# Optimization experiments

Hardware: AMD Instinct MI355X
Metric: run time of the kernel (lower is better)

## Reference

```python
import jax, jax.numpy as jnp
import numpy as np
import math

DIM, H, Q_RANK, KV_RANK = 2048, 16, 768, 512
QK_STATIC, QK_ROT, V_DIM = 128, 64, 128
QK_TOTAL = QK_STATIC + QK_ROT
BS, SEQ = 2, 1024


def rmsnorm(x, scale, eps=1e-6):
    xf = x.astype(jnp.float32)
    return scale * (xf * jax.lax.rsqrt(jnp.mean(xf * xf, axis=-1, keepdims=True) + eps))


def half_rotate(x):
    h = x.shape[-1] // 2
    return jnp.concatenate([-x[..., h:], x[..., :h]], axis=-1)


def rope_tables(seq_len, dim):
    inv_freq = 1.0 / (10000.0 ** (jnp.arange(0, dim, 2, dtype=jnp.float32) / dim))
    freqs = jnp.arange(seq_len, dtype=jnp.float32)[:, None] * inv_freq[None, :]
    cos = jnp.concatenate([jnp.cos(freqs), jnp.cos(freqs)], axis=-1)  # (S, dim)
    sin = jnp.concatenate([jnp.sin(freqs), jnp.sin(freqs)], axis=-1)
    return cos, sin


def setup_inputs() -> dict:
    key = jax.random.key(0)
    ks = jax.random.split(key, 10)
    sc = lambda fan_in: 1.0 / math.sqrt(fan_in)
    x = jax.random.normal(ks[0], (BS, SEQ, DIM), dtype=jnp.float32)
    causal = jnp.where(jnp.tril(jnp.ones((SEQ, SEQ), dtype=bool)), 0.0, -1e9).astype(jnp.float32)
    mask = jnp.broadcast_to(causal[None], (BS, SEQ, SEQ))
    return {
        "x": x,
        "start_pos": 0,
        "mask": mask,
        "q_down_w": jax.random.normal(ks[1], (Q_RANK, DIM)) * sc(DIM),
        "q_down_b": jnp.zeros((Q_RANK,), jnp.float32),
        "q_norm_scale": jnp.ones((Q_RANK,), jnp.float32),
        "q_up_w": jax.random.normal(ks[2], (H * QK_TOTAL, Q_RANK)) * sc(Q_RANK),
        "q_up_b": jnp.zeros((H * QK_TOTAL,), jnp.float32),
        "kv_down_w": jax.random.normal(ks[3], (KV_RANK + QK_ROT, DIM)) * sc(DIM),
        "kv_down_b": jnp.zeros((KV_RANK + QK_ROT,), jnp.float32),
        "kv_norm_scale": jnp.ones((KV_RANK,), jnp.float32),
        "kv_up_w": jax.random.normal(ks[4], (H * (QK_STATIC + V_DIM), KV_RANK)) * sc(KV_RANK),
        "out_w": jax.random.normal(ks[5], (DIM, H * V_DIM)) * sc(H * V_DIM),
        "out_b": jnp.zeros((DIM,), jnp.float32),
    }


def reference(x, start_pos, mask, q_down_w, q_down_b, q_norm_scale, q_up_w, q_up_b,
              kv_down_w, kv_down_b, kv_norm_scale, kv_up_w, out_w, out_b):
    bs, seq_len, _ = x.shape
    # q path: down-proj -> RMSNorm -> up-proj
    q = rmsnorm(x @ q_down_w.T + q_down_b, q_norm_scale)
    q = (q @ q_up_w.T + q_up_b).reshape(bs, seq_len, H, QK_TOTAL)
    q_static, q_rot = q[..., :QK_STATIC], q[..., QK_STATIC:]
    # kv path: shared down-proj producing latent features + rotary key part
    kv = x @ kv_down_w.T + kv_down_b
    kv_feat, k_rot = kv[..., :KV_RANK], kv[..., KV_RANK:]
    # RoPE (original indexes positions 0..seq_len-1)
    cos, sin = rope_tables(seq_len, QK_ROT)
    q_rot = q_rot * cos[None, :, None, :] + half_rotate(q_rot) * sin[None, :, None, :]
    k_rot = k_rot * cos[None, :, :] + half_rotate(k_rot) * sin[None, :, :]  # (b, t, r)
    kv_normed = rmsnorm(kv_feat, kv_norm_scale)  # latent cache contents (b, t, c)
    # matrix absorption: fold kv_up key-weights into q
    w_k_abs = kv_up_w[: H * QK_STATIC, :].reshape(H, QK_STATIC, KV_RANK)
    w_v_abs = kv_up_w[-H * V_DIM :, :].reshape(H, V_DIM, KV_RANK)
    q_static_proj = jnp.einsum('bshd,hdc->bshc', q_static, w_k_abs)
    attn_scores = (jnp.einsum('bshc,btc->bsht', q_static_proj, kv_normed)
                   + jnp.einsum('bshr,btr->bsht', q_rot, k_rot)) / math.sqrt(QK_TOTAL)
    attn_scores = attn_scores + mask[:, :, None, :]
    attn_weights = jax.nn.softmax(attn_scores, axis=-1)
    # attend over latent features, then expand with absorbed value weights
    ctx_c = jnp.einsum('bsht,btc->bshc', attn_weights, kv_normed)
    ctx = jnp.einsum('bshc,hdc->bshd', ctx_c, w_v_abs)
    out = ctx.reshape(bs, seq_len, H * V_DIM) @ out_w.T + out_b
    return out
```

## Files before the change

kernel.cpp:

```cpp
#include <hip/hip_runtime.h>
#include <stdint.h>
#include <stddef.h>


typedef __attribute__((ext_vector_type(8))) short bf16x8;
typedef __attribute__((ext_vector_type(4))) float f32x4;

__device__ inline float b2f(unsigned short v){
    union { unsigned u; float f; } x; x.u = ((unsigned)v) << 16; return x.f;
}
__device__ inline unsigned short f2b(float f){
    union { float f; unsigned u; } x; x.f = f;
    unsigned r = x.u + 0x7fffu + ((x.u >> 16) & 1u);
    return (unsigned short)(r >> 16);
}
__device__ inline float tofloat(float v){ return v; }
__device__ inline float tofloat(unsigned short v){ return b2f(v); }

__device__ __forceinline__ void gl2lds16(const unsigned short* g, unsigned short* l){
    __builtin_amdgcn_global_load_lds(
        (__attribute__((address_space(1))) void*)const_cast<unsigned short*>(g),
        (__attribute__((address_space(3))) void*)l,
        16, 0, 0);
}

template<typename TC>
__global__ __launch_bounds__(256) void mfma_gemm_bt(
    const unsigned short* __restrict__ A, const unsigned short* __restrict__ B,
    const float* __restrict__ bias, TC* __restrict__ C,
    int M, int N, int K, int lda, int ldb, int ldc,
    int zdiv, long sA_hi, long sA_lo, long sB_hi, long sB_lo, long sC_hi, long sC_lo,
    float alpha, int causal)
{
    int z, bm, bn;
    if (causal & 4){ z = blockIdx.x; bm = blockIdx.y; bn = blockIdx.z; }
    else           { z = blockIdx.z; bm = blockIdx.y; bn = blockIdx.x; }
    int m0, n0;
    if (causal & 1){
        int i = bm;
        int mt = (int)((sqrtf(8.f * i + 1.f) - 1.f) * 0.5f);
        while ((mt + 1) * (mt + 2) / 2 <= i) ++mt;
        while (mt * (mt + 1) / 2 > i) --mt;
        n0 = (i - mt * (mt + 1) / 2) * 128;
        m0 = mt * 128;
    } else { m0 = bm * 128; n0 = bn * 128; }
    if (causal & 2) K = min(K, m0 + 128);

    __shared__ unsigned short As[3][4096];
    __shared__ unsigned short Bs[3][4096];
    const int zh = z / zdiv, zl = z % zdiv;
    A += (size_t)zh * sA_hi + (size_t)zl * sA_lo;
    B += (size_t)zh * sB_hi + (size_t)zl * sB_lo;
    C += (size_t)zh * sC_hi + (size_t)zl * sC_lo;

    const int tid = threadIdx.x, w = tid >> 6, lane = tid & 63;
    const int wm = w >> 1, wn = w & 1;

    const int srow = w * 32 + (lane >> 2);
    const int schunk = ((lane & 3) ^ ((lane >> 3) & 3)) * 8;
    const unsigned short* gA = A + (size_t)(m0 + srow) * lda + schunk;
    const unsigned short* gB = B + (size_t)(n0 + srow) * ldb + schunk;

    const int ktiles = K >> 5;
    auto stage = [&](int buf, int kt){
        const int k0 = kt << 5;
        gl2lds16(gA + k0,            &As[buf][w * 1024]);
        gl2lds16(gA + k0 + 16 * lda, &As[buf][w * 1024 + 512]);
        gl2lds16(gB + k0,            &Bs[buf][w * 1024]);
        gl2lds16(gB + k0 + 16 * ldb, &Bs[buf][w * 1024 + 512]);
    };
    stage(0, 0);
    if (ktiles > 1) stage(1, 1);

    f32x4 acc[4][4] = {};
    const int lm = lane & 15;
    const int kq = (((lane >> 4) ^ (lm >> 1)) & 3) * 8;

    int cur = 0;
    for (int kt = 0; kt < ktiles; ++kt){
        if (kt + 1 < ktiles) __builtin_amdgcn_s_waitcnt(0xF74);
        else                 __builtin_amdgcn_s_waitcnt(0xF70);
        __builtin_amdgcn_s_barrier();
        __asm__ volatile("" ::: "memory");
        if (kt + 2 < ktiles) stage(cur >= 1 ? cur - 1 : 2, kt + 2);
        bf16x8 af[4], bfr[4];
        #pragma unroll
        for (int i = 0; i < 4; ++i)
            af[i] = *(const bf16x8*)&As[cur][(wm * 64 + i * 16 + lm) * 32 + kq];
        #pragma unroll
        for (int j = 0; j < 4; ++j)
            bfr[j] = *(const bf16x8*)&Bs[cur][(wn * 64 + j * 16 + lm) * 32 + kq];
        #pragma unroll
        for (int i = 0; i < 4; ++i)
            #pragma unroll
            for (int j = 0; j < 4; ++j)
                acc[i][j] = __builtin_amdgcn_mfma_f32_16x16x32_bf16(af[i], bfr[j], acc[i][j], 0, 0, 0);
        __asm__ volatile("" ::: "memory");
        cur = (cur == 2) ? 0 : cur + 1;
    }

    #pragma unroll
    for (int i = 0; i < 4; ++i){
        const int m = m0 + wm * 64 + i * 16 + (lane >> 4) * 4;
        #pragma unroll
        for (int j = 0; j < 4; ++j){
            const int n = n0 + wn * 64 + j * 16 + lm;
            if (n < N){
                const float bb = bias ? bias[n] : 0.f;
                #pragma unroll
                for (int r = 0; r < 4; ++r){
                    float v = acc[i][j][r] * alpha + bb;
                    if ((causal & 1) && n > m + r) v = -1e9f;
                    if constexpr (sizeof(TC) == 2)
                        C[(size_t)(m + r) * ldc + n] = (TC)f2b(v);
                    else
                        C[(size_t)(m + r) * ldc + n] = (TC)v;
                }
            }
        }
    }
}

__global__ __launch_bounds__(256) void flash_attn(
    const unsigned short* __restrict__ qcat,
    const unsigned short* __restrict__ kcat,
    const unsigned short* __restrict__ vhT,
    unsigned short* __restrict__ ctx)
{
    const int z = blockIdx.x;
    const int mt = 15 - (int)blockIdx.y;
    const int b = z >> 4, h = z & 15;
    const int m0 = mt * 64;
    const int nkt = (mt >> 1) + 1;

    __shared__ char smem[74240];
    unsigned short (*Qs)[4096] = (unsigned short (*)[4096])smem;
    unsigned short (*Ks)[8192] = (unsigned short (*)[8192])(smem + 24576);
    unsigned short* Ps = (unsigned short*)smem;
    float* lrow = (float*)(smem + 73728);

    const unsigned short* qA = qcat + ((size_t)b * 16384 + h) * 576;
    const unsigned short* kB = kcat + (size_t)b * 589824;
    const unsigned short* vB = vhT + (size_t)z * 131072;

    const int tid = threadIdx.x, w = tid >> 6, lane = tid & 63;
    const int wm = w >> 1, wn = w & 1;
    const int lm = lane & 15, g = lane >> 4;
    const int kq = g * 8;
    const int rs7 = lm & 7;

    if (tid < 128) lrow[tid] = 0.f;

    const int srow8 = lane >> 3;
    const int soff8 = ((lane & 7) ^ (lane >> 3)) * 8;
    const unsigned short* gQ = qA + (size_t)(m0 + w * 16 + srow8) * 9216 + soff8;

    f32x4 Oacc[2][4] = {};
    const float scl = 0.07216878364870322f;

    for (int kt = 0; kt < nkt; ++kt){
        bf16x8 vfr[4][4];
        #pragma unroll
        for (int j = 0; j < 4; ++j)
            #pragma unroll
            for (int kc = 0; kc < 4; ++kc)
                vfr[j][kc] = *(const bf16x8*)(vB + (size_t)(wn * 64 + j * 16 + lm) * 1024
                                              + kt * 128 + kc * 32 + kq);

        const unsigned short* gK = kB + (size_t)(kt * 128 + w * 32 + srow8) * 576 + soff8;
        auto stageQK = [&](int buf, int c){
            const int k0 = c * 64;
            gl2lds16(gQ + k0,             &Qs[buf][w * 1024]);
            gl2lds16(gQ + k0 + 8 * 9216,  &Qs[buf][w * 1024 + 512]);
            gl2lds16(gK + k0,             &Ks[buf][w * 2048]);
            gl2lds16(gK + k0 + 8 * 576,   &Ks[buf][w * 2048 + 512]);
            gl2lds16(gK + k0 + 16 * 576,  &Ks[buf][w * 2048 + 1024]);
            gl2lds16(gK + k0 + 24 * 576,  &Ks[buf][w * 2048 + 1536]);
        };
        stageQK(0, 0);
        stageQK(1, 1);

        f32x4 S[2][4] = {};
        int cur = 0;
        for (int c = 0; c < 9; ++c){
            if (c < 8) __builtin_amdgcn_s_waitcnt(0xF76);
            else       __builtin_amdgcn_s_waitcnt(0xF70);
            __builtin_amdgcn_s_barrier();
            __asm__ volatile("" ::: "memory");
            if (c + 2 < 9) stageQK(cur >= 1 ? cur - 1 : 2, c + 2);
            bf16x8 af[2][2], bfr[4][2];
            #pragma unroll
            for (int i = 0; i < 2; ++i)
                #pragma unroll
                for (int kk = 0; kk < 2; ++kk)
                    af[i][kk] = *(const bf16x8*)&Qs[cur][(wm * 32 + i * 16 + lm) * 64
                                                         + (((kk * 4 + g) ^ rs7) * 8)];
            #pragma unroll
            for (int j = 0; j < 4; ++j)
                #pragma unroll
                for (int kk = 0; kk < 2; ++kk)
                    bfr[j][kk] = *(const bf16x8*)&Ks[cur][(wn * 64 + j * 16 + lm) * 64
                                                          + (((kk * 4 + g) ^ rs7) * 8)];
            #pragma unroll
            for (int kk = 0; kk < 2; ++kk)
                #pragma unroll
                for (int i = 0; i < 2; ++i)
                    #pragma unroll
                    for (int j = 0; j < 4; ++j)
                        S[i][j] = __builtin_amdgcn_mfma_f32_16x16x32_bf16(af[i][kk], bfr[j][kk], S[i][j], 0, 0, 0);
            __asm__ volatile("" ::: "memory");
            cur = (cur == 2) ? 0 : cur + 1;
        }
        __syncthreads();

        const bool diag = (kt == (mt >> 1));
        #pragma unroll
        for (int i = 0; i < 2; ++i){
            float rs[4] = {0.f, 0.f, 0.f, 0.f};
            #pragma unroll
            for (int j = 0; j < 4; ++j){
                const int nloc = wn * 64 + j * 16 + lm;
                #pragma unroll
                for (int r = 0; r < 4; ++r){
                    const int mloc = wm * 32 + i * 16 + g * 4 + r;
                    float p = __expf(S[i][j][r] * scl);
                    if (diag && (kt * 128 + nloc) > (m0 + mloc)) p = 0.f;
                    rs[r] += p;
                    Ps[mloc * 136 + nloc] = f2b(p);
                }
            }
            #pragma unroll
            for (int r = 0; r < 4; ++r){
                rs[r] += __shfl_xor(rs[r], 1, 64);
                rs[r] += __shfl_xor(rs[r], 2, 64);
                rs[r] += __shfl_xor(rs[r], 4, 64);
                rs[r] += __shfl_xor(rs[r], 8, 64);
            }
            if (lm == 0){
                #pragma unroll
                for (int r = 0; r < 4; ++r)
                    lrow[wn * 64 + wm * 32 + i * 16 + g * 4 + r] += rs[r];
            }
        }
        __syncthreads();

        #pragma unroll
        for (int kc = 0; kc < 4; ++kc){
            bf16x8 pa[2];
            #pragma unroll
            for (int i = 0; i < 2; ++i)
                pa[i] = *(const bf16x8*)&Ps[(wm * 32 + i * 16 + lm) * 136 + kc * 32 + kq];
            #pragma unroll
            for (int i = 0; i < 2; ++i)
                #pragma unroll
                for (int j = 0; j < 4; ++j)
                    Oacc[i][j] = __builtin_amdgcn_mfma_f32_16x16x32_bf16(pa[i], vfr[j][kc], Oacc[i][j], 0, 0, 0);
        }
        __syncthreads();
    }

    unsigned short* cBase = ctx + ((size_t)(b * 1024 + m0)) * 2048 + h * 128;
    #pragma unroll
    for (int i = 0; i < 2; ++i){
        #pragma unroll
        for (int r = 0; r < 4; ++r){
            const int row = wm * 32 + i * 16 + g * 4 + r;
            const float inv = 1.f / (lrow[row] + lrow[64 + row]);
            #pragma unroll
            for (int j = 0; j < 4; ++j){
                const int col = wn * 64 + j * 16 + lm;
                cBase[(size_t)row * 2048 + col] = f2b(Oacc[i][j][r] * inv);
            }
        }
    }
}

__global__ __launch_bounds__(256) void cast_all(
    const float* __restrict__ s0, unsigned short* __restrict__ d0,
    const float* __restrict__ s1, unsigned short* __restrict__ d1,
    const float* __restrict__ s2, unsigned short* __restrict__ d2,
    const float* __restrict__ s3, unsigned short* __restrict__ d3,
    const float* __restrict__ s4, unsigned short* __restrict__ d4,
    const float* __restrict__ s5, unsigned short* __restrict__ d5)
{
    long i = (long)(blockIdx.x * 256 + threadIdx.x) * 4;
    const float* s; unsigned short* d; long off;
    if      (i <  4194304L){ s = s0; d = d0; off = i; }
    else if (i <  5767168L){ s = s1; d = d1; off = i -  4194304L; }
    else if (i <  8126464L){ s = s2; d = d2; off = i -  5767168L; }
    else if (i <  9306112L){ s = s3; d = d3; off = i -  8126464L; }
    else if (i < 11403264L){ s = s4; d = d4; off = i -  9306112L; }
    else                   { s = s5; d = d5; off = i - 11403264L; }
    float4 v = *(const float4*)(s + off);
    *(ushort4*)(d + off) = make_ushort4(f2b(v.x), f2b(v.y), f2b(v.z), f2b(v.w));
}

template<typename TIn>
__global__ __launch_bounds__(256) void transpose_to_bf16(
    const TIn* __restrict__ in, unsigned short* __restrict__ out,
    int ldin, int R, long sZin, long sZout)
{
    __shared__ float t[32][33];
    const int z = blockIdx.z;
    in  += (size_t)z * sZin;
    out += (size_t)z * sZout;
    const int r0 = blockIdx.y * 32, c0 = blockIdx.x * 32;
    const int tx = threadIdx.x & 31, ty = threadIdx.x >> 5;
    #pragma unroll
    for (int rr = ty; rr < 32; rr += 8)
        t[rr][tx] = tofloat(in[(size_t)(r0 + rr) * ldin + c0 + tx]);
    __syncthreads();
    #pragma unroll
    for (int cc = ty; cc < 32; cc += 8)
        out[(size_t)(c0 + cc) * R + r0 + tx] = f2b(t[tx][cc]);
}

__global__ __launch_bounds__(256) void fused_down_post(
    const unsigned short* __restrict__ p,
    const float* __restrict__ q_down_b, const float* __restrict__ kv_down_b,
    const float* __restrict__ q_norm_s, const float* __restrict__ kv_norm_s,
    unsigned short* __restrict__ qn, unsigned short* __restrict__ kcat)
{
    __shared__ float row[1344];
    __shared__ float red[4];
    const int t = blockIdx.x, tid = threadIdx.x;
    const long S = 2752512L;
    const unsigned short* b0 = p + (size_t)t * 1344;
    for (int c = tid; c < 1344; c += 256){
        float v = b2f(b0[c]) + b2f(b0[c + S]) + b2f(b0[c + 2*S]) + b2f(b0[c + 3*S]);
        v += (c < 768) ? q_down_b[c] : kv_down_b[c - 768];
        row[c] = v;
    }
    __syncthreads();
    const int lane = tid & 63, w = tid >> 6;
    float ss = 0.f;
    for (int c = tid; c < 768; c += 256){ float v = row[c]; ss += v * v; }
    #pragma unroll
    for (int o = 32; o > 0; o >>= 1) ss += __shfl_xor(ss, o, 64);
    if (lane == 0) red[w] = ss;
    __syncthreads();
    const float inv1 = rsqrtf((red[0]+red[1]+red[2]+red[3]) / 768.f + 1e-6f);
    __syncthreads();
    ss = 0.f;
    for (int c = tid; c < 512; c += 256){ float v = row[768 + c]; ss += v * v; }
    #pragma unroll
    for (int o = 32; o > 0; o >>= 1) ss += __shfl_xor(ss, o, 64);
    if (lane == 0) red[w] = ss;
    __syncthreads();
    const float inv2 = rsqrtf((red[0]+red[1]+red[2]+red[3]) / 512.f + 1e-6f);
    for (int c = tid; c < 768; c += 256)
        qn[(size_t)t * 768 + c] = f2b(q_norm_s[c] * row[c] * inv1);
    for (int c = tid; c < 512; c += 256)
        kcat[(size_t)t * 576 + c] = f2b(kv_norm_s[c] * row[768 + c] * inv2);
    if (tid < 64){
        const int d = tid, s = t & 1023;
        float x  = row[1280 + d];
        float xp = (d < 32) ? -row[1280 + d + 32] : row[1280 + d - 32];
        float ang = (float)s * powf(10000.f, -(float)(2 * (d & 31)) / 64.f);
        kcat[(size_t)t * 576 + 512 + d] = f2b(x * cosf(ang) + xp * sinf(ang));
    }
}

__global__ __launch_bounds__(256) void reduce_out(
    const unsigned short* __restrict__ p, const float* __restrict__ bias,
    float* __restrict__ out)
{
    const long S = 4194304L;
    long i = (long)(blockIdx.x * 256 + threadIdx.x) * 4;
    ushort4 a = *(const ushort4*)(p + i);
    ushort4 b = *(const ushort4*)(p + i + S);
    float4 bb = *(const float4*)(bias + (i & 2047));
    float4 r = make_float4(b2f(a.x) + b2f(b.x) + bb.x, b2f(a.y) + b2f(b.y) + bb.y,
                           b2f(a.z) + b2f(b.z) + bb.z, b2f(a.w) + b2f(b.w) + bb.w);
    *(float4*)(out + i) = r;
}

__global__ __launch_bounds__(256) void q_rope_kernel(const unsigned short* __restrict__ qu,
                                                     unsigned short* __restrict__ qcat)
{
    const int idx = blockIdx.x * 256 + threadIdx.x;
    const int d   = idx & 63;
    const int h   = (idx >> 6) & 15;
    const int tok = idx >> 10;
    const int s   = tok & 1023;
    const unsigned short* base = qu + (size_t)tok * 3072 + h * 192 + 128;
    float x  = b2f(base[d]);
    float xp = (d < 32) ? -b2f(base[d + 32]) : b2f(base[d - 32]);
    float ang = (float)s * powf(10000.f, -(float)(2 * (d & 31)) / 64.f);
    qcat[((size_t)tok * 16 + h) * 576 + 512 + d] = f2b(x * cosf(ang) + xp * sinf(ang));
}

extern "C" void kernel_launch(void* const* d_in, const int* in_sizes, int n_in,
                              void* d_out, int out_size, void* d_ws, size_t ws_size,
                              hipStream_t stream)
{
    const float* x         = (const float*)d_in[0];
    const float* q_down_w  = (const float*)d_in[3];
    const float* q_down_b  = (const float*)d_in[4];
    const float* q_norm_s  = (const float*)d_in[5];
    const float* q_up_w    = (const float*)d_in[6];
    const float* q_up_b    = (const float*)d_in[7];
    const float* kv_down_w = (const float*)d_in[8];
    const float* kv_down_b = (const float*)d_in[9];
    const float* kv_norm_s = (const float*)d_in[10];
    const float* kv_up_w   = (const float*)d_in[11];
    const float* out_w     = (const float*)d_in[12];
    const float* out_b     = (const float*)d_in[13];
    float* out = (float*)d_out;

    char* ws = (char*)d_ws;
    unsigned short* kvuw  = (unsigned short*)(ws + 0);
    unsigned short* outw  = (unsigned short*)(ws + 4194304);
    unsigned short* wkT   = (unsigned short*)(ws + 12582912);
    unsigned short* kcat  = (unsigned short*)(ws + 14680064);
    unsigned short* vhT   = (unsigned short*)(ws + 17039360);
    unsigned short* qcat  = (unsigned short*)(ws + 25427968);
    unsigned short* ctx   = (unsigned short*)(ws + 63176704);
    unsigned short* qu    = (unsigned short*)(ws + 71565312);
    unsigned short* qn    = (unsigned short*)(ws + 84148224);
    unsigned short* p_out = (unsigned short*)(ws + 71565312);
    unsigned short* p_qkv = (unsigned short*)(ws + 88342528);
    unsigned short* xb    = (unsigned short*)(ws + 110362624);
    unsigned short* qkdw  = (unsigned short*)(ws + 118751232);
    unsigned short* quw   = (unsigned short*)(ws + 124518400);

    dim3 blk(256);

    cast_all<<<15232, blk, 0, stream>>>(x, xb, q_down_w, qkdw, q_up_w, quw,
                                        kv_down_w, qkdw + 1572864, kv_up_w, kvuw, out_w, outw);
    transpose_to_bf16<float><<<dim3(16, 4, 16), blk, 0, stream>>>(
        kv_up_w, wkT, 512, 128, 65536L, 65536L);

    mfma_gemm_bt<unsigned short><<<dim3(11, 16, 4), blk, 0, stream>>>(
        xb, qkdw, nullptr, p_qkv, 2048, 1344, 512, 2048, 2048, 1344,
        4, 0L, 512L, 0L, 512L, 0L, 2752512L, 1.0f, 0);
    fused_down_post<<<2048, blk, 0, stream>>>(p_qkv, q_down_b, kv_down_b,
                                              q_norm_s, kv_norm_s, qn, kcat);
    mfma_gemm_bt<unsigned short><<<dim3(24, 16, 1), blk, 0, stream>>>(
        qn, quw, q_up_b, qu, 2048, 3072, 768, 768, 768, 3072,
        1, 0, 0, 0, 0, 0, 0, 1.0f, 0);
    mfma_gemm_bt<unsigned short><<<dim3(32, 1, 8), blk, 0, stream>>>(
        kvuw + 1048576, kcat, nullptr, vhT, 128, 1024, 512, 512, 576, 1024,
        16, 0L, 65536L, 589824L, 0L, 2097152L, 131072L, 1.0f, 4);
    q_rope_kernel<<<8192, blk, 0, stream>>>(qu, qcat);
    mfma_gemm_bt<unsigned short><<<dim3(16, 16, 4), blk, 0, stream>>>(
        qu, wkT, nullptr, qcat, 2048, 512, 128, 3072, 128, 9216,
        16, 0, 192L, 0, 65536L, 0, 576L, 1.0f, 4);
    flash_attn<<<dim3(32, 16), blk, 0, stream>>>(qcat, kcat, vhT, ctx);
    mfma_gemm_bt<unsigned short><<<dim3(16, 16, 2), blk, 0, stream>>>(
        ctx, outw, nullptr, p_out, 2048, 2048, 1024, 2048, 2048, 2048,
        2, 0L, 1024L, 0L, 1024L, 0L, 4194304L, 1.0f, 0);
    reduce_out<<<4096, blk, 0, stream>>>(p_out, out_b, out);
}
```

Measured before the change: 339.1 us.

## Un-absorb key weights: expand per-head K instead of projecting Q to latent

Instead of folding the key up-projection into Q (512-wide latent scores per head), the code now computes per-head keys K_h = kv_normed · W_k^T (128 dims) and concatenates the rotary part, so attention QK uses 192-dim dot products instead of 576. Q is read directly from the up-projection output with RoPE applied in place, and its three 64-wide chunks are loaded into LDS once per block rather than restaged every key tile. This removes the transpose kernel and the Q-absorption GEMM and cuts the QK MFMA work by about a third. In exchange it adds a per-head K expansion GEMM and a larger per-head key buffer, and the P tile now lives in the K staging region.

Measured after the change: 309.4 us. -8.8%, faster.

```diff
diff --git a/kernel.cpp b/kernel.cpp
--- a/kernel.cpp
+++ b/kernel.cpp
@@ -14,8 +14,6 @@
     unsigned r = x.u + 0x7fffu + ((x.u >> 16) & 1u);
     return (unsigned short)(r >> 16);
 }
-__device__ inline float tofloat(float v){ return v; }
-__device__ inline float tofloat(unsigned short v){ return b2f(v); }
 
 __device__ __forceinline__ void gl2lds16(const unsigned short* g, unsigned short* l){
     __builtin_amdgcn_global_load_lds(
@@ -122,8 +120,8 @@
 }
 
 __global__ __launch_bounds__(256) void flash_attn(
-    const unsigned short* __restrict__ qcat,
-    const unsigned short* __restrict__ kcat,
+    const unsigned short* __restrict__ qu,
+    const unsigned short* __restrict__ khcat,
     const unsigned short* __restrict__ vhT,
     unsigned short* __restrict__ ctx)
 {
@@ -136,11 +134,10 @@
     __shared__ char smem[74240];
     unsigned short (*Qs)[4096] = (unsigned short (*)[4096])smem;
     unsigned short (*Ks)[8192] = (unsigned short (*)[8192])(smem + 24576);
-    unsigned short* Ps = (unsigned short*)smem;
+    unsigned short* Ps = (unsigned short*)(smem + 24576);
     float* lrow = (float*)(smem + 73728);
 
-    const unsigned short* qA = qcat + ((size_t)b * 16384 + h) * 576;
-    const unsigned short* kB = kcat + (size_t)b * 589824;
+    const unsigned short* kB = khcat + (size_t)z * 196608;
     const unsigned short* vB = vhT + (size_t)z * 131072;
 
     const int tid = threadIdx.x, w = tid >> 6, lane = tid & 63;
@@ -153,7 +150,14 @@
 
     const int srow8 = lane >> 3;
     const int soff8 = ((lane & 7) ^ (lane >> 3)) * 8;
-    const unsigned short* gQ = qA + (size_t)(m0 + w * 16 + srow8) * 9216 + soff8;
+    const unsigned short* gQ = qu + (size_t)(b * 1024 + m0 + w * 16 + srow8) * 3072
+                               + h * 192 + soff8;
+
+    #pragma unroll
+    for (int c = 0; c < 3; ++c){
+        gl2lds16(gQ + c * 64,            &Qs[c][w * 1024]);
+        gl2lds16(gQ + c * 64 + 8 * 3072, &Qs[c][w * 1024 + 512]);
+    }
 
     f32x4 Oacc[2][4] = {};
     const float scl = 0.07216878364870322f;
@@ -167,40 +171,38 @@
                 vfr[j][kc] = *(const bf16x8*)(vB + (size_t)(wn * 64 + j * 16 + lm) * 1024
                                               + kt * 128 + kc * 32 + kq);
 
-        const unsigned short* gK = kB + (size_t)(kt * 128 + w * 32 + srow8) * 576 + soff8;
-        auto stageQK = [&](int buf, int c){
+        const unsigned short* gK = kB + (size_t)(kt * 128 + w * 32 + srow8) * 192 + soff8;
+        auto stageK = [&](int buf, int c){
             const int k0 = c * 64;
-            gl2lds16(gQ + k0,             &Qs[buf][w * 1024]);
-            gl2lds16(gQ + k0 + 8 * 9216,  &Qs[buf][w * 1024 + 512]);
-            gl2lds16(gK + k0,             &Ks[buf][w * 2048]);
-            gl2lds16(gK + k0 + 8 * 576,   &Ks[buf][w * 2048 + 512]);
-            gl2lds16(gK + k0 + 16 * 576,  &Ks[buf][w * 2048 + 1024]);
-            gl2lds16(gK + k0 + 24 * 576,  &Ks[buf][w * 2048 + 1536]);
+            gl2lds16(gK + k0,            &Ks[buf][w * 2048]);
+            gl2lds16(gK + k0 + 8 * 192,  &Ks[buf][w * 2048 + 512]);
+            gl2lds16(gK + k0 + 16 * 192, &Ks[buf][w * 2048 + 1024]);
+            gl2lds16(gK + k0 + 24 * 192, &Ks[buf][w * 2048 + 1536]);
         };
-        stageQK(0, 0);
-        stageQK(1, 1);
+        stageK(0, 0);
+        stageK(1, 1);
 
         f32x4 S[2][4] = {};
-        int cur = 0;
-        for (int c = 0; c < 9; ++c){
-            if (c < 8) __builtin_amdgcn_s_waitcnt(0xF76);
+        #pragma unroll
+        for (int c = 0; c < 3; ++c){
+            if (c < 2) __builtin_amdgcn_s_waitcnt(0xF74);
             else       __builtin_amdgcn_s_waitcnt(0xF70);
             __builtin_amdgcn_s_barrier();
             __asm__ volatile("" ::: "memory");
-            if (c + 2 < 9) stageQK(cur >= 1 ? cur - 1 : 2, c + 2);
+            if (c == 0) stageK(2, 2);
             bf16x8 af[2][2], bfr[4][2];
             #pragma unroll
             for (int i = 0; i < 2; ++i)
                 #pragma unroll
                 for (int kk = 0; kk < 2; ++kk)
-                    af[i][kk] = *(const bf16x8*)&Qs[cur][(wm * 32 + i * 16 + lm) * 64
-                                                         + (((kk * 4 + g) ^ rs7) * 8)];
+                    af[i][kk] = *(const bf16x8*)&Qs[c][(wm * 32 + i * 16 + lm) * 64
+                                                       + (((kk * 4 + g) ^ rs7) * 8)];
             #pragma unroll
             for (int j = 0; j < 4; ++j)
                 #pragma unroll
                 for (int kk = 0; kk < 2; ++kk)
-                    bfr[j][kk] = *(const bf16x8*)&Ks[cur][(wn * 64 + j * 16 + lm) * 64
-                                                          + (((kk * 4 + g) ^ rs7) * 8)];
+                    bfr[j][kk] = *(const bf16x8*)&Ks[c][(wn * 64 + j * 16 + lm) * 64
+                                                        + (((kk * 4 + g) ^ rs7) * 8)];
             #pragma unroll
             for (int kk = 0; kk < 2; ++kk)
                 #pragma unroll
@@ -209,7 +211,6 @@
                     for (int j = 0; j < 4; ++j)
                         S[i][j] = __builtin_amdgcn_mfma_f32_16x16x32_bf16(af[i][kk], bfr[j][kk], S[i][j], 0, 0, 0);
             __asm__ volatile("" ::: "memory");
-            cur = (cur == 2) ? 0 : cur + 1;
         }
         __syncthreads();
 
@@ -293,26 +294,6 @@
     else                   { s = s5; d = d5; off = i - 11403264L; }
     float4 v = *(const float4*)(s + off);
     *(ushort4*)(d + off) = make_ushort4(f2b(v.x), f2b(v.y), f2b(v.z), f2b(v.w));
-}
-
-template<typename TIn>
-__global__ __launch_bounds__(256) void transpose_to_bf16(
-    const TIn* __restrict__ in, unsigned short* __restrict__ out,
-    int ldin, int R, long sZin, long sZout)
-{
-    __shared__ float t[32][33];
-    const int z = blockIdx.z;
-    in  += (size_t)z * sZin;
-    out += (size_t)z * sZout;
-    const int r0 = blockIdx.y * 32, c0 = blockIdx.x * 32;
-    const int tx = threadIdx.x & 31, ty = threadIdx.x >> 5;
-    #pragma unroll
-    for (int rr = ty; rr < 32; rr += 8)
-        t[rr][tx] = tofloat(in[(size_t)(r0 + rr) * ldin + c0 + tx]);
-    __syncthreads();
-    #pragma unroll
-    for (int cc = ty; cc < 32; cc += 8)
-        out[(size_t)(c0 + cc) * R + r0 + tx] = f2b(t[tx][cc]);
 }
 
 __global__ __launch_bounds__(256) void fused_down_post(
@@ -375,19 +356,32 @@
     *(float4*)(out + i) = r;
 }
 
-__global__ __launch_bounds__(256) void q_rope_kernel(const unsigned short* __restrict__ qu,
-                                                     unsigned short* __restrict__ qcat)
-{
-    const int idx = blockIdx.x * 256 + threadIdx.x;
-    const int d   = idx & 63;
-    const int h   = (idx >> 6) & 15;
-    const int tok = idx >> 10;
-    const int s   = tok & 1023;
-    const unsigned short* base = qu + (size_t)tok * 3072 + h * 192 + 128;
-    float x  = b2f(base[d]);
-    float xp = (d < 32) ? -b2f(base[d + 32]) : b2f(base[d - 32]);
-    float ang = (float)s * powf(10000.f, -(float)(2 * (d & 31)) / 64.f);
-    qcat[((size_t)tok * 16 + h) * 576 + 512 + d] = f2b(x * cosf(ang) + xp * sinf(ang));
+__global__ __launch_bounds__(256) void rope_q_krot(
+    unsigned short* __restrict__ qu,
+    const unsigned short* __restrict__ kcat,
+    unsigned short* __restrict__ khcat)
+{
+    long idx = (long)blockIdx.x * 256 + threadIdx.x;
+    if (idx < 1048576L){
+        const int d   = idx & 31;
+        const int h   = (idx >> 5) & 15;
+        const int tok = idx >> 9;
+        const int s   = tok & 1023;
+        unsigned short* base = qu + (size_t)tok * 3072 + h * 192 + 128;
+        float x1 = b2f(base[d]), x2 = b2f(base[d + 32]);
+        float ang = (float)s * powf(10000.f, -(float)d / 32.f);
+        float c = cosf(ang), sn = sinf(ang);
+        base[d]      = f2b(x1 * c - x2 * sn);
+        base[d + 32] = f2b(x2 * c + x1 * sn);
+    } else {
+        idx -= 1048576L;
+        const int d   = idx & 63;
+        const int h   = (idx >> 6) & 15;
+        const int tok = (int)(idx >> 10);
+        const int bb  = tok >> 10, s = tok & 1023;
+        khcat[((size_t)(bb * 16 + h) * 1024 + s) * 192 + 128 + d] =
+            kcat[(size_t)tok * 576 + 512 + d];
+    }
 }
 
 extern "C" void kernel_launch(void* const* d_in, const int* in_sizes, int n_in,
@@ -411,25 +405,22 @@
     char* ws = (char*)d_ws;
     unsigned short* kvuw  = (unsigned short*)(ws + 0);
     unsigned short* outw  = (unsigned short*)(ws + 4194304);
-    unsigned short* wkT   = (unsigned short*)(ws + 12582912);
-    unsigned short* kcat  = (unsigned short*)(ws + 14680064);
-    unsigned short* vhT   = (unsigned short*)(ws + 17039360);
-    unsigned short* qcat  = (unsigned short*)(ws + 25427968);
-    unsigned short* ctx   = (unsigned short*)(ws + 63176704);
-    unsigned short* qu    = (unsigned short*)(ws + 71565312);
-    unsigned short* qn    = (unsigned short*)(ws + 84148224);
-    unsigned short* p_out = (unsigned short*)(ws + 71565312);
-    unsigned short* p_qkv = (unsigned short*)(ws + 88342528);
-    unsigned short* xb    = (unsigned short*)(ws + 110362624);
-    unsigned short* qkdw  = (unsigned short*)(ws + 118751232);
-    unsigned short* quw   = (unsigned short*)(ws + 124518400);
+    unsigned short* kcat  = (unsigned short*)(ws + 12582912);
+    unsigned short* vhT   = (unsigned short*)(ws + 14942208);
+    unsigned short* khcat = (unsigned short*)(ws + 23330816);
+    unsigned short* ctx   = (unsigned short*)(ws + 35913728);
+    unsigned short* qu    = (unsigned short*)(ws + 44302336);
+    unsigned short* qn    = (unsigned short*)(ws + 56885248);
+    unsigned short* p_qkv = (unsigned short*)(ws + 60030976);
+    unsigned short* p_out = (unsigned short*)(ws + 60030976);
+    unsigned short* xb    = (unsigned short*)(ws + 82051072);
+    unsigned short* qkdw  = (unsigned short*)(ws + 90439680);
+    unsigned short* quw   = (unsigned short*)(ws + 96206848);
 
     dim3 blk(256);
 
     cast_all<<<15232, blk, 0, stream>>>(x, xb, q_down_w, qkdw, q_up_w, quw,
                                         kv_down_w, qkdw + 1572864, kv_up_w, kvuw, out_w, outw);
-    transpose_to_bf16<float><<<dim3(16, 4, 16), blk, 0, stream>>>(
-        kv_up_w, wkT, 512, 128, 65536L, 65536L);
 
     mfma_gemm_bt<unsigned short><<<dim3(11, 16, 4), blk, 0, stream>>>(
         xb, qkdw, nullptr, p_qkv, 2048, 1344, 512, 2048, 2048, 1344,
@@ -442,11 +433,11 @@
     mfma_gemm_bt<unsigned short><<<dim3(32, 1, 8), blk, 0, stream>>>(
         kvuw + 1048576, kcat, nullptr, vhT, 128, 1024, 512, 512, 576, 1024,
         16, 0L, 65536L, 589824L, 0L, 2097152L, 131072L, 1.0f, 4);
-    q_rope_kernel<<<8192, blk, 0, stream>>>(qu, qcat);
-    mfma_gemm_bt<unsigned short><<<dim3(16, 16, 4), blk, 0, stream>>>(
-        qu, wkT, nullptr, qcat, 2048, 512, 128, 3072, 128, 9216,
-        16, 0, 192L, 0, 65536L, 0, 576L, 1.0f, 4);
-    flash_attn<<<dim3(32, 16), blk, 0, stream>>>(qcat, kcat, vhT, ctx);
+    mfma_gemm_bt<unsigned short><<<dim3(32, 8, 1), blk, 0, stream>>>(
+        kcat, kvuw, nullptr, khcat, 1024, 128, 512, 576, 512, 192,
+        16, 589824L, 0L, 0L, 65536L, 3145728L, 196608L, 1.0f, 4);
+    rope_q_krot<<<12288, blk, 0, stream>>>(qu, kcat, khcat);
+    flash_attn<<<dim3(32, 16), blk, 0, stream>>>(qu, khcat, vhT, ctx);
     mfma_gemm_bt<unsigned short><<<dim3(16, 16, 2), blk, 0, stream>>>(
         ctx, outw, nullptr, p_out, 2048, 2048, 1024, 2048, 2048, 2048,
         2, 0L, 1024L, 0L, 1024L, 0L, 4194304L, 1.0f, 0);
```
